# Kernel optimization log

Measured on AMD Instinct MI355X. Metric: run time of the kernel, lower is better.

The kernel has to match this reference:

```python
import jax, jax.numpy as jnp
import numpy as np

F = 32          # features
L2 = 16         # (max_degree+1)^2 spherical components, max_degree=3
K = 16          # num radial basis functions
CUTOFF = 6.0
GAMMA = 1.0
NZ = 119        # max_atomic_number + 1
KE = 14.399645  # Coulomb constant, eV*Angstrom
ZBL_C = np.array([0.18175, 0.50986, 0.28022, 0.02817], dtype=np.float32)
ZBL_D = np.array([3.19980, 0.94229, 0.40290, 0.20162], dtype=np.float32)


def _smooth_cutoff(r):
    u = jnp.minimum(r / CUTOFF, 1.0 - 1e-6)
    return jnp.where(r < CUTOFF, jnp.exp(-u * u / (1.0 - u * u)), 0.0)


def _radial(r):
    # exponential-Chebyshev radial basis: T_k(2*exp(-gamma*r)-1), k=0..K-1
    t = jnp.clip(2.0 * jnp.exp(-GAMMA * r) - 1.0, -1.0, 1.0)
    ks = jnp.arange(K, dtype=jnp.float32)
    return jnp.cos(ks[None, :] * jnp.arccos(t)[:, None])  # (E,K)


def _sph_harm(u):
    # real spherical harmonics up to l=3 on unit vectors u (E,3) -> (E,16)
    x, y, z = u[:, 0], u[:, 1], u[:, 2]
    x2, y2, z2 = x * x, y * y, z * z
    return jnp.stack([
        jnp.full_like(x, 0.282095),
        0.488603 * y, 0.488603 * z, 0.488603 * x,
        1.092548 * x * y, 1.092548 * y * z, 0.315392 * (3.0 * z2 - 1.0),
        1.092548 * x * z, 0.546274 * (x2 - y2),
        0.590044 * y * (3.0 * x2 - y2), 2.890611 * x * y * z,
        0.457046 * y * (5.0 * z2 - 1.0), 0.373176 * z * (5.0 * z2 - 3.0),
        0.457046 * x * (5.0 * z2 - 1.0), 1.445306 * z * (x2 - y2),
        0.590044 * x * (x2 - 3.0 * y2),
    ], axis=-1)


def setup_inputs() -> dict:
    key = jax.random.key(0)
    ks = jax.random.split(key, 16)
    N, E, B = 16384, 262144, 512
    atomic_numbers = jax.random.randint(ks[0], (N,), 0, 18)
    positions = jax.random.normal(ks[1], (N, 3), dtype=jnp.float32) * 3.0
    dst_idx = jax.random.randint(ks[2], (E,), 0, N)
    src_idx = jax.random.randint(ks[3], (E,), 0, N)
    batch_segments = jnp.sort(jax.random.randint(ks[4], (N,), 0, B))
    p = lambda k, shp, s: jax.random.normal(k, shp, dtype=jnp.float32) * s
    return {
        "atomic_numbers": atomic_numbers,
        "positions": positions,
        "dst_idx": dst_idx,
        "src_idx": src_idx,
        "batch_segments": batch_segments,
        "batch_size": B,
        "batch_mask": jnp.ones((B,), dtype=jnp.float32),
        "atom_mask": jnp.ones((N,), dtype=jnp.float32),
        "embed": p(ks[5], (NZ, F), 0.1),
        "Wr1_0": p(ks[6], (K, F), 0.25),
        "Wr2_0": p(ks[7], (K, F), 0.25),
        "W1_0": p(ks[8], (F, F), 0.18),
        "W2_0": p(ks[9], (F, F), 0.18),
        "Wr1_1": p(ks[10], (K, F), 0.25),
        "W1_1": p(ks[11], (F, F), 0.18),
        "W2_1": p(ks[12], (F, F), 0.18),
        "w_out": p(ks[13], (F,), 0.1),
        "b_out": p(ks[14], (NZ,), 0.1),
    }


def reference(atomic_numbers, positions, dst_idx, src_idx, batch_segments,
              batch_size, batch_mask, atom_mask, embed,
              Wr1_0, Wr2_0, W1_0, W2_0, Wr1_1, W1_1, W2_1, w_out, b_out):
    N = positions.shape[0]
    # ---- geometric features (gather on edges) ----
    disp = positions[src_idx] - positions[dst_idx]          # (E,3)
    r = jnp.sqrt(jnp.sum(disp * disp, axis=-1) + 1e-10)     # (E,)
    r = jnp.maximum(r, 1e-4)
    cut = _smooth_cutoff(r)                                  # (E,)
    rad = _radial(r) * cut[:, None]                          # (E,K)
    sh = _sph_harm(disp / r[:, None])                        # (E,L2)

    # ---- atom embedding lifted to equivariant features (N,L2,F) ----
    x = jnp.zeros((N, L2, F), dtype=jnp.float32).at[:, 0, :].set(embed[atomic_numbers])

    # ---- iteration 0: full-degree message passing ----
    g1 = rad @ Wr1_0                                         # (E,F) scalar->tensor path
    g2 = rad @ Wr2_0                                         # (E,F) degree-preserving path
    xs = x[src_idx]                                          # (E,L2,F)
    m = sh[:, :, None] * (g1[:, None, :] * xs[:, 0:1, :]) + g2[:, None, :] * xs
    x = jax.ops.segment_sum(m, dst_idx, num_segments=N)      # (N,L2,F)
    # refinement (equivariant gated residual MLP)
    h = jnp.einsum('nlf,fg->nlg', x, W1_0)
    x = x + jnp.einsum('nlf,fg->nlg', h * jax.nn.silu(h[:, 0:1, :]), W2_0)

    # ---- iteration 1: max_degree=0 message passing ----
    x0 = x[:, 0, :]                                          # (N,F)
    g = rad @ Wr1_1                                          # (E,F)
    x0 = jax.ops.segment_sum(g * x0[src_idx], dst_idx, num_segments=N)
    x0 = x0 + jax.nn.silu(x0 @ W1_1) @ W2_1                  # scalar refinement

    # ---- atomic energy readout ----
    e_atom = x0 @ w_out + b_out[atomic_numbers]              # (N,)

    # ---- ZBL nuclear repulsion over edges ----
    zf = atomic_numbers.astype(jnp.float32)
    zd, zs = zf[dst_idx], zf[src_idx]
    a = 0.8854 * 0.529177 / (zd ** 0.23 + zs ** 0.23 + 1e-10)
    phi = jnp.sum(ZBL_C[None, :] * jnp.exp(-ZBL_D[None, :] * (r / a)[:, None]), axis=-1)
    e_pair = 0.5 * KE * zd * zs / r * phi * cut
    e_atom = e_atom + jax.ops.segment_sum(e_pair, dst_idx, num_segments=N)

    e_atom = e_atom * atom_mask
    # scatter atomic energies to molecules
    e_mol = jax.ops.segment_sum(e_atom, batch_segments, num_segments=batch_size)
    return e_mol * batch_mask                                # (B,)
```

## Files before the change

### kernel.cpp

```cpp
#include <hip/hip_runtime.h>
#include <hip/hip_fp16.h>


#define FDIM 32
#define KDIM 16
#define BINCAP 32
#define MAXZ 18

__device__ __forceinline__ int pack_ct(float cut, float tt) {
    unsigned lo = __half_as_ushort(__float2half_rn(cut));
    unsigned hi = __half_as_ushort(__float2half_rn(tt));
    return (int)((hi << 16) | lo);
}
__device__ __forceinline__ float unpack_cut(int w) {
    return __half2float(__ushort_as_half((unsigned short)(w & 0xFFFF)));
}
__device__ __forceinline__ float unpack_tt(int w) {
    return __half2float(__ushort_as_half((unsigned short)(((unsigned)w) >> 16)));
}

__global__ __launch_bounds__(256) void edge_k(
    const int* __restrict__ dst, const int* __restrict__ src,
    const int* __restrict__ Z, const float* __restrict__ pos,
    int* __restrict__ counts, float* __restrict__ pair,
    int2* __restrict__ bins, int E)
{
    __shared__ float zpow[MAXZ];
    int tid = threadIdx.x;
    if (tid < MAXZ) zpow[tid] = __powf((float)tid, 0.23f);
    __syncthreads();

    int base = (blockIdx.x * 256 + tid) * 4;
    if (base >= E) return;
    int4 d4 = *(const int4*)(dst + base);
    int4 s4 = *(const int4*)(src + base);
    #pragma unroll
    for (int jj = 0; jj < 4; ++jj) {
        int d = (&d4.x)[jj], s = (&s4.x)[jj];
        float dx = pos[3 * s]     - pos[3 * d];
        float dy = pos[3 * s + 1] - pos[3 * d + 1];
        float dz = pos[3 * s + 2] - pos[3 * d + 2];
        float r2 = dx * dx + dy * dy + dz * dz;
        if (r2 >= 36.0f) continue;
        float r = fmaxf(sqrtf(r2 + 1e-10f), 1e-4f);
        float u = r * (1.0f / 6.0f);
        float u2 = u * u;
        float cut = __expf(-u2 / (1.0f - u2));
        float tt = fminf(fmaxf(2.0f * __expf(-r) - 1.0f, -1.0f), 1.0f);
        int zs_i = Z[s], zd_i = Z[d];
        float zd = (float)zd_i, zsf = (float)zs_i;
        float zsum = zpow[zd_i] + zpow[zs_i] + 1e-10f;
        float ra = r * zsum * (1.0f / 0.46853312f);
        float phi = 0.18175f * __expf(-3.1998f  * ra)
                  + 0.50986f * __expf(-0.94229f * ra)
                  + 0.28022f * __expf(-0.4029f  * ra)
                  + 0.02817f * __expf(-0.20162f * ra);
        atomicAdd(&pair[d], 0.5f * 14.399645f * zd * zsf / r * phi * cut);
        int slot = atomicAdd(&counts[d], 1);
        if (slot < BINCAP)
            bins[d * BINCAP + slot] = make_int2(s | (zs_i << 14), pack_ct(cut, tt));
    }
}

__global__ __launch_bounds__(256) void gather1_k(
    const int* __restrict__ counts, const int2* __restrict__ bins,
    const float* __restrict__ embed, const float* __restrict__ Wr1_0,
    const float* __restrict__ Wr2_0, const float* __restrict__ W1_0,
    const float* __restrict__ W2_0, float* __restrict__ x0, int N)
{
    __shared__ float Wc[KDIM * FDIM];
    __shared__ float W1s[FDIM * FDIM];
    __shared__ float W2s[FDIM * FDIM];
    __shared__ float emb_s[MAXZ * FDIM];
    int tid = threadIdx.x;
    for (int i = tid; i < KDIM * FDIM; i += 256)
        Wc[i] = 0.282095f * Wr1_0[i] + Wr2_0[i];
    for (int i = tid; i < FDIM * FDIM; i += 256) { W1s[i] = W1_0[i]; W2s[i] = W2_0[i]; }
    for (int i = tid; i < MAXZ * FDIM; i += 256) emb_s[i] = embed[i];
    __syncthreads();

    int a = (blockIdx.x * 256 + tid) >> 6;
    if (a >= N) return;
    int lane = tid & 63;
    int j = lane >> 5, f = lane & 31;
    int rv = ((const int*)(bins + (size_t)a * BINCAP))[lane];
    int deg = min(counts[a], BINCAP);
    float acc = 0.f;
    for (int i = j; i < deg; i += 2) {
        int w0 = __shfl(rv, 2 * i);
        int w1 = __shfl(rv, 2 * i + 1);
        int zs = (w0 >> 14) & 31;
        float cut = unpack_cut(w1), tt = unpack_tt(w1);
        float T0 = 1.0f, T1 = tt;
        float gc = Wc[f] + Wc[FDIM + f] * tt;
        #pragma unroll
        for (int k = 2; k < KDIM; ++k) {
            float T2 = 2.0f * tt * T1 - T0;
            gc = fmaf(Wc[k * FDIM + f], T2, gc);
            T0 = T1; T1 = T2;
        }
        acc = fmaf(cut * gc, emb_s[zs * FDIM + f], acc);
    }
    acc += __shfl_down(acc, 32);
    float h = 0.f;
    #pragma unroll
    for (int g = 0; g < FDIM; ++g)
        h = fmaf(__shfl(acc, g, 32), W1s[g * FDIM + f], h);
    float cc = h * h / (1.0f + __expf(-h));
    float xo = acc;
    #pragma unroll
    for (int g = 0; g < FDIM; ++g)
        xo = fmaf(__shfl(cc, g, 32), W2s[g * FDIM + f], xo);
    if (lane < 32) x0[(size_t)a * FDIM + f] = xo;
}

__global__ __launch_bounds__(256) void gather2_k(
    const int* __restrict__ counts, const int2* __restrict__ bins,
    const float* __restrict__ x0, const float* __restrict__ pair,
    const float* __restrict__ Wr1_1, const float* __restrict__ W1_1,
    const float* __restrict__ W2_1, const float* __restrict__ w_out,
    const float* __restrict__ b_out, const int* __restrict__ Z,
    const int* __restrict__ bseg, const float* __restrict__ bmask,
    const float* __restrict__ amask, float* __restrict__ out, int N)
{
    __shared__ float Wg[KDIM * FDIM];
    __shared__ float W1s[FDIM * FDIM];
    __shared__ float W2s[FDIM * FDIM];
    __shared__ float wo[FDIM];
    int tid = threadIdx.x;
    for (int i = tid; i < KDIM * FDIM; i += 256) Wg[i] = Wr1_1[i];
    for (int i = tid; i < FDIM * FDIM; i += 256) { W1s[i] = W1_1[i]; W2s[i] = W2_1[i]; }
    if (tid < FDIM) wo[tid] = w_out[tid];
    __syncthreads();

    int a = (blockIdx.x * 256 + tid) >> 6;
    if (a >= N) return;
    int lane = tid & 63;
    int j = lane >> 5, f = lane & 31;
    int rv = ((const int*)(bins + (size_t)a * BINCAP))[lane];
    int deg = min(counts[a], BINCAP);
    float acc = 0.f;
    int i = j;
    float xv = 0.f; int w1 = 0;
    if (i < deg) {
        int w0 = __shfl(rv, 2 * i);
        w1 = __shfl(rv, 2 * i + 1);
        xv = x0[(size_t)(w0 & 0x3FFF) * FDIM + f];
    }
    while (i < deg) {
        int inext = i + 2;
        float xv_n = 0.f; int w1_n = 0;
        if (inext < deg) {
            int w0n = __shfl(rv, 2 * inext);
            w1_n = __shfl(rv, 2 * inext + 1);
            xv_n = x0[(size_t)(w0n & 0x3FFF) * FDIM + f];
        }
        float cut = unpack_cut(w1), tt = unpack_tt(w1);
        float T0 = 1.0f, T1 = tt;
        float gr = Wg[f] + Wg[FDIM + f] * tt;
        #pragma unroll
        for (int k = 2; k < KDIM; ++k) {
            float T2 = 2.0f * tt * T1 - T0;
            gr = fmaf(Wg[k * FDIM + f], T2, gr);
            T0 = T1; T1 = T2;
        }
        acc = fmaf(cut * gr, xv, acc);
        i = inext; w1 = w1_n; xv = xv_n;
    }
    acc += __shfl_down(acc, 32);
    float h = 0.f;
    #pragma unroll
    for (int g = 0; g < FDIM; ++g)
        h = fmaf(__shfl(acc, g, 32), W1s[g * FDIM + f], h);
    float cc = h / (1.0f + __expf(-h));
    float xo = acc;
    #pragma unroll
    for (int g = 0; g < FDIM; ++g)
        xo = fmaf(__shfl(cc, g, 32), W2s[g * FDIM + f], xo);
    float ea = xo * wo[f];
    #pragma unroll
    for (int m = 16; m >= 1; m >>= 1) ea += __shfl_xor(ea, m, 32);
    if (lane == 0) {
        float e_atom = ea + b_out[Z[a]] + pair[a];
        int b = bseg[a];
        atomicAdd(&out[b], e_atom * amask[a] * bmask[b]);
    }
}

extern "C" void kernel_launch(void* const* d_in, const int* in_sizes, int n_in,
                              void* d_out, int out_size, void* d_ws, size_t ws_size,
                              hipStream_t stream) {
    int N = in_sizes[0];
    int E = in_sizes[2];
    int B = in_sizes[6];

    const int*   Z      = (const int*)d_in[0];
    const float* pos    = (const float*)d_in[1];
    const int*   dst    = (const int*)d_in[2];
    const int*   src    = (const int*)d_in[3];
    const int*   bseg   = (const int*)d_in[4];
    const float* bmask  = (const float*)d_in[6];
    const float* amask  = (const float*)d_in[7];
    const float* embed  = (const float*)d_in[8];
    const float* Wr1_0  = (const float*)d_in[9];
    const float* Wr2_0  = (const float*)d_in[10];
    const float* W1_0   = (const float*)d_in[11];
    const float* W2_0   = (const float*)d_in[12];
    const float* Wr1_1  = (const float*)d_in[13];
    const float* W1_1   = (const float*)d_in[14];
    const float* W2_1   = (const float*)d_in[15];
    const float* w_out  = (const float*)d_in[16];
    const float* b_out  = (const float*)d_in[17];
    float* out = (float*)d_out;

    int2*  bins   = (int2*)d_ws;
    int*   counts = (int*)(bins + (size_t)N * BINCAP);
    float* pair   = (float*)(counts + N);
    float* x0     = pair + N;

    hipMemsetAsync(counts, 0, (size_t)2 * N * sizeof(int), stream);
    hipMemsetAsync(out, 0, (size_t)B * sizeof(float), stream);

    int eb = (E / 4 + 255) / 256;
    edge_k<<<eb, 256, 0, stream>>>(dst, src, Z, pos, counts, pair, bins, E);

    int gb = (N * 64 + 255) / 256;
    gather1_k<<<gb, 256, 0, stream>>>(counts, bins, embed, Wr1_0, Wr2_0,
                                      W1_0, W2_0, x0, N);
    gather2_k<<<gb, 256, 0, stream>>>(counts, bins, x0, pair, Wr1_1, W1_1, W2_1,
                                      w_out, b_out, Z, bseg, bmask, amask, out, N);
}
```

Before: 169.9 us.

## Map two atoms per wavefront in gather kernels with two-edge unrolled loop

Both gather kernels now give each 32-lane half-wave its own atom, instead of splitting one atom's edges across the two halves. This halves the launch size and removes the cross-half reduction and the duplicated 32x32 MLP work. The edge loop processes two edges per iteration, reading bin entries directly from memory and masking invalid ones. This adds independent Chebyshev chains and gathers in flight for more instruction-level parallelism. The cost is divergence when the paired atoms have unequal degrees, plus wasted reads of padded bin slots.

```diff
diff --git a/kernel.cpp b/kernel.cpp
--- a/kernel.cpp
+++ b/kernel.cpp
@@ -79,29 +79,38 @@
     for (int i = tid; i < MAXZ * FDIM; i += 256) emb_s[i] = embed[i];
     __syncthreads();
 
-    int a = (blockIdx.x * 256 + tid) >> 6;
+    int w = (blockIdx.x * 256 + tid) >> 6;
+    int lane = tid & 63, f = lane & 31;
+    int a = 2 * w + (lane >> 5);
     if (a >= N) return;
-    int lane = tid & 63;
-    int j = lane >> 5, f = lane & 31;
-    int rv = ((const int*)(bins + (size_t)a * BINCAP))[lane];
     int deg = min(counts[a], BINCAP);
+    int dm = max(__shfl(deg, 0), __shfl(deg, 32));
+    const int2* row = bins + (size_t)a * BINCAP;
     float acc = 0.f;
-    for (int i = j; i < deg; i += 2) {
-        int w0 = __shfl(rv, 2 * i);
-        int w1 = __shfl(rv, 2 * i + 1);
-        int zs = (w0 >> 14) & 31;
-        float cut = unpack_cut(w1), tt = unpack_tt(w1);
-        float T0 = 1.0f, T1 = tt;
-        float gc = Wc[f] + Wc[FDIM + f] * tt;
+    for (int i = 0; i < dm; i += 2) {
+        int2 r0 = row[i];
+        int2 r1 = row[i + 1];
+        bool v0 = i < deg, v1 = (i + 1) < deg;
+        float c0 = v0 ? unpack_cut(r0.y) : 0.f;
+        float c1 = v1 ? unpack_cut(r1.y) : 0.f;
+        int z0 = v0 ? ((r0.x >> 14) & 31) : 0;
+        int z1 = v1 ? ((r1.x >> 14) & 31) : 0;
+        float t0 = unpack_tt(r0.y), t1 = unpack_tt(r1.y);
+        float A0 = 1.f, A1 = t0, B0 = 1.f, B1 = t1;
+        float g0 = Wc[f] + Wc[FDIM + f] * t0;
+        float g1 = Wc[f] + Wc[FDIM + f] * t1;
         #pragma unroll
         for (int k = 2; k < KDIM; ++k) {
-            float T2 = 2.0f * tt * T1 - T0;
-            gc = fmaf(Wc[k * FDIM + f], T2, gc);
-            T0 = T1; T1 = T2;
+            float A2 = 2.f * t0 * A1 - A0;
+            float B2 = 2.f * t1 * B1 - B0;
+            float wk = Wc[k * FDIM + f];
+            g0 = fmaf(wk, A2, g0);
+            g1 = fmaf(wk, B2, g1);
+            A0 = A1; A1 = A2; B0 = B1; B1 = B2;
         }
-        acc = fmaf(cut * gc, emb_s[zs * FDIM + f], acc);
-    }
-    acc += __shfl_down(acc, 32);
+        acc = fmaf(c0 * g0, emb_s[z0 * FDIM + f], acc);
+        acc = fmaf(c1 * g1, emb_s[z1 * FDIM + f], acc);
+    }
     float h = 0.f;
     #pragma unroll
     for (int g = 0; g < FDIM; ++g)
@@ -111,7 +120,7 @@
     #pragma unroll
     for (int g = 0; g < FDIM; ++g)
         xo = fmaf(__shfl(cc, g, 32), W2s[g * FDIM + f], xo);
-    if (lane < 32) x0[(size_t)a * FDIM + f] = xo;
+    x0[(size_t)a * FDIM + f] = xo;
 }
 
 __global__ __launch_bounds__(256) void gather2_k(
@@ -133,41 +142,40 @@
     if (tid < FDIM) wo[tid] = w_out[tid];
     __syncthreads();
 
-    int a = (blockIdx.x * 256 + tid) >> 6;
+    int w = (blockIdx.x * 256 + tid) >> 6;
+    int lane = tid & 63, f = lane & 31;
+    int a = 2 * w + (lane >> 5);
     if (a >= N) return;
-    int lane = tid & 63;
-    int j = lane >> 5, f = lane & 31;
-    int rv = ((const int*)(bins + (size_t)a * BINCAP))[lane];
     int deg = min(counts[a], BINCAP);
+    int dm = max(__shfl(deg, 0), __shfl(deg, 32));
+    const int2* row = bins + (size_t)a * BINCAP;
     float acc = 0.f;
-    int i = j;
-    float xv = 0.f; int w1 = 0;
-    if (i < deg) {
-        int w0 = __shfl(rv, 2 * i);
-        w1 = __shfl(rv, 2 * i + 1);
-        xv = x0[(size_t)(w0 & 0x3FFF) * FDIM + f];
-    }
-    while (i < deg) {
-        int inext = i + 2;
-        float xv_n = 0.f; int w1_n = 0;
-        if (inext < deg) {
-            int w0n = __shfl(rv, 2 * inext);
-            w1_n = __shfl(rv, 2 * inext + 1);
-            xv_n = x0[(size_t)(w0n & 0x3FFF) * FDIM + f];
-        }
-        float cut = unpack_cut(w1), tt = unpack_tt(w1);
-        float T0 = 1.0f, T1 = tt;
-        float gr = Wg[f] + Wg[FDIM + f] * tt;
+    for (int i = 0; i < dm; i += 2) {
+        int2 r0 = row[i];
+        int2 r1 = row[i + 1];
+        bool v0 = i < deg, v1 = (i + 1) < deg;
+        int s0 = v0 ? (r0.x & 0x3FFF) : 0;
+        int s1 = v1 ? (r1.x & 0x3FFF) : 0;
+        float xa = x0[(size_t)s0 * FDIM + f];
+        float xb = x0[(size_t)s1 * FDIM + f];
+        float c0 = v0 ? unpack_cut(r0.y) : 0.f;
+        float c1 = v1 ? unpack_cut(r1.y) : 0.f;
+        float t0 = unpack_tt(r0.y), t1 = unpack_tt(r1.y);
+        float A0 = 1.f, A1 = t0, B0 = 1.f, B1 = t1;
+        float g0 = Wg[f] + Wg[FDIM + f] * t0;
+        float g1 = Wg[f] + Wg[FDIM + f] * t1;
         #pragma unroll
         for (int k = 2; k < KDIM; ++k) {
-            float T2 = 2.0f * tt * T1 - T0;
-            gr = fmaf(Wg[k * FDIM + f], T2, gr);
-            T0 = T1; T1 = T2;
+            float A2 = 2.f * t0 * A1 - A0;
+            float B2 = 2.f * t1 * B1 - B0;
+            float wk = Wg[k * FDIM + f];
+            g0 = fmaf(wk, A2, g0);
+            g1 = fmaf(wk, B2, g1);
+            A0 = A1; A1 = A2; B0 = B1; B1 = B2;
         }
-        acc = fmaf(cut * gr, xv, acc);
-        i = inext; w1 = w1_n; xv = xv_n;
-    }
-    acc += __shfl_down(acc, 32);
+        acc = fmaf(c0 * g0, xa, acc);
+        acc = fmaf(c1 * g1, xb, acc);
+    }
     float h = 0.f;
     #pragma unroll
     for (int g = 0; g < FDIM; ++g)
@@ -180,7 +188,7 @@
     float ea = xo * wo[f];
     #pragma unroll
     for (int m = 16; m >= 1; m >>= 1) ea += __shfl_xor(ea, m, 32);
-    if (lane == 0) {
+    if ((lane & 31) == 0) {
         float e_atom = ea + b_out[Z[a]] + pair[a];
         int b = bseg[a];
         atomicAdd(&out[b], e_atom * amask[a] * bmask[b]);
@@ -224,7 +232,7 @@
     int eb = (E / 4 + 255) / 256;
     edge_k<<<eb, 256, 0, stream>>>(dst, src, Z, pos, counts, pair, bins, E);
 
-    int gb = (N * 64 + 255) / 256;
+    int gb = (N / 2 * 64 + 255) / 256;
     gather1_k<<<gb, 256, 0, stream>>>(counts, bins, embed, Wr1_0, Wr2_0,
                                       W1_0, W2_0, x0, N);
     gather2_k<<<gb, 256, 0, stream>>>(counts, bins, x0, pair, Wr1_1, W1_1, W2_1,
```

Measured after the change: 149.7 us. 11.9% less time.
